# Optimization experiments

Hardware: AMD Instinct MI355X
Metric: run time of the kernel (lower is better)

The kernel has to match this reference:

```python
import jax, jax.numpy as jnp
import numpy as np

T = 8192          # nb_territories
H = 4096          # hidden_size
N_ACT = 65536     # number of possible (orig, dest) action pairs
NEG = -1000.0     # fill value for masked-out actions (matches torch code)


def setup_inputs() -> dict:
    key = jax.random.key(0)
    ks = jax.random.split(key, 8)
    inv_sqrt = lambda n: 1.0 / np.sqrt(n)
    return {
        "possible_actions": jax.random.randint(ks[0], (N_ACT, 2), 0, T, dtype=jnp.int64)
            if jax.config.jax_enable_x64 else jax.random.randint(ks[0], (N_ACT, 2), 0, T, dtype=jnp.int32),
        "player_presence_map": jax.random.normal(ks[1], (T,), dtype=jnp.float32),
        "W_in": jax.random.normal(ks[2], (H, T), dtype=jnp.float32) * inv_sqrt(T),
        "b_in": jax.random.normal(ks[3], (H,), dtype=jnp.float32) * inv_sqrt(T),
        "W_orig": jax.random.normal(ks[4], (T, H), dtype=jnp.float32) * inv_sqrt(H),
        "b_orig": jax.random.normal(ks[5], (T,), dtype=jnp.float32) * inv_sqrt(H),
        "W_dest": jax.random.normal(ks[6], (T, H), dtype=jnp.float32) * inv_sqrt(H),
        "b_dest": jax.random.normal(ks[7], (T,), dtype=jnp.float32) * inv_sqrt(H),
    }


def reference(possible_actions, player_presence_map, W_in, b_in, W_orig, b_orig, W_dest, b_dest):
    # tiny MLP: x = tanh(Linear(presence)); torig/tdest heads
    x = jnp.tanh(W_in @ player_presence_map + b_in)          # [H]
    torig = jnp.tanh(W_orig @ x + b_orig)                    # [T]
    tdest = jnp.tanh(W_dest @ x + b_dest)                    # [T]
    emb = jnp.outer(torig, tdest)                            # [T, T]
    # vectorized scatter replaces the python loop over possible_actions
    mask = jnp.zeros((T, T), dtype=emb.dtype)
    mask = mask.at[possible_actions[:, 0], possible_actions[:, 1]].set(1.0)
    emb = jnp.where(mask == 1.0, emb, jnp.asarray(NEG, emb.dtype))
    logits = emb.reshape(1, T * T)                           # [1, T*T]
    return jax.nn.softmax(logits, axis=1)
```

## Files before the change

kernel.cpp:

```cpp
#include <hip/hip_runtime.h>

constexpr int TT   = 8192;
constexpr int HH   = 4096;
constexpr int NACT = 65536;

__global__ __launch_bounds__(256) void k_gemv_in(
    const float* __restrict__ W, const float* __restrict__ p,
    const float* __restrict__ b, float* __restrict__ x)
{
    const int row = blockIdx.x;
    const int t   = threadIdx.x;
    const float4* __restrict__ Wr = reinterpret_cast<const float4*>(W + (size_t)row * TT);
    const float4* __restrict__ pv = reinterpret_cast<const float4*>(p);
    float acc = 0.f;
#pragma unroll
    for (int i = 0; i < TT / 4 / 256; ++i) {
        float4 w = Wr[i * 256 + t];
        float4 q = pv[i * 256 + t];
        acc += w.x * q.x + w.y * q.y + w.z * q.z + w.w * q.w;
    }
#pragma unroll
    for (int off = 32; off; off >>= 1) acc += __shfl_down(acc, off, 64);
    __shared__ float s[4];
    if ((t & 63) == 0) s[t >> 6] = acc;
    __syncthreads();
    if (t == 0) x[row] = tanhf(s[0] + s[1] + s[2] + s[3] + b[row]);
}

__global__ __launch_bounds__(256) void k_gemv_heads(
    const float* __restrict__ Wo, const float* __restrict__ bo,
    const float* __restrict__ Wd, const float* __restrict__ bd,
    const float* __restrict__ x, float* __restrict__ th)
{
    const int bid = blockIdx.x;
    const int t   = threadIdx.x;
    const float* W; const float* b; int r;
    if (bid < TT) { W = Wo; b = bo; r = bid; }
    else          { W = Wd; b = bd; r = bid - TT; }
    const float4* __restrict__ Wr = reinterpret_cast<const float4*>(W + (size_t)r * HH);
    const float4* __restrict__ xv = reinterpret_cast<const float4*>(x);
    float acc = 0.f;
#pragma unroll
    for (int i = 0; i < HH / 4 / 256; ++i) {
        float4 w = Wr[i * 256 + t];
        float4 q = xv[i * 256 + t];
        acc += w.x * q.x + w.y * q.y + w.z * q.z + w.w * q.w;
    }
#pragma unroll
    for (int off = 32; off; off >>= 1) acc += __shfl_down(acc, off, 64);
    __shared__ float s[4];
    if ((t & 63) == 0) s[t >> 6] = acc;
    __syncthreads();
    if (t == 0) th[bid] = tanhf(s[0] + s[1] + s[2] + s[3] + b[r]);
}

__global__ __launch_bounds__(256) void k_scatter(
    const int* __restrict__ pa, const float* __restrict__ th,
    float* __restrict__ out, float* __restrict__ partial)
{
    const int i = blockIdx.x * 256 + threadIdx.x;
    const int o = pa[2 * i];
    const int d = pa[2 * i + 1];
    const float v = th[o] * th[TT + d];
    const float u = expf(v - 1.0f);
    float old = atomicExch(out + ((size_t)o * TT + d), u);
    float c = (old == 0.0f) ? u : 0.0f;
#pragma unroll
    for (int off = 32; off; off >>= 1) c += __shfl_down(c, off, 64);
    __shared__ float s[4];
    if ((threadIdx.x & 63) == 0) s[threadIdx.x >> 6] = c;
    __syncthreads();
    if (threadIdx.x == 0) partial[blockIdx.x] = s[0] + s[1] + s[2] + s[3];
}

__global__ __launch_bounds__(256) void k_finalize(
    const int* __restrict__ pa, const float* __restrict__ th,
    const float* __restrict__ partial, float* __restrict__ out)
{
    float ps = partial[threadIdx.x];
#pragma unroll
    for (int off = 32; off; off >>= 1) ps += __shfl_down(ps, off, 64);
    __shared__ float s[4];
    __shared__ float invZ;
    if ((threadIdx.x & 63) == 0) s[threadIdx.x >> 6] = ps;
    __syncthreads();
    if (threadIdx.x == 0) invZ = 1.0f / (s[0] + s[1] + s[2] + s[3]);
    __syncthreads();
    const int i = blockIdx.x * 256 + threadIdx.x;
    const int o = pa[2 * i];
    const int d = pa[2 * i + 1];
    const float v = th[o] * th[TT + d];
    out[(size_t)o * TT + d] = expf(v - 1.0f) * invZ;
}

extern "C" void kernel_launch(void* const* d_in, const int* in_sizes, int n_in,
                              void* d_out, int out_size, void* d_ws, size_t ws_size,
                              hipStream_t stream)
{
    const int*   pa  = (const int*)  d_in[0];
    const float* p   = (const float*)d_in[1];
    const float* Win = (const float*)d_in[2];
    const float* bin = (const float*)d_in[3];
    const float* Wo  = (const float*)d_in[4];
    const float* bo  = (const float*)d_in[5];
    const float* Wd  = (const float*)d_in[6];
    const float* bd  = (const float*)d_in[7];
    float* out = (float*)d_out;

    float* x       = (float*)d_ws;
    float* th      = x + HH;
    float* partial = th + 2 * TT;

    hipMemsetAsync(out, 0, (size_t)out_size * sizeof(float), stream);

    k_gemv_in   <<<HH,        256, 0, stream>>>(Win, p, bin, x);
    k_gemv_heads<<<2 * TT,    256, 0, stream>>>(Wo, bo, Wd, bd, x, th);
    k_scatter   <<<NACT / 256, 256, 0, stream>>>(pa, th, out, partial);
    k_finalize  <<<NACT / 256, 256, 0, stream>>>(pa, th, partial, out);
}
```

Baseline: 144.7 us.

## Fuse all stages into one cooperative persistent kernel with grid syncs

Replaces the memset and four kernel launches with a single cooperative kernel that runs each stage in grid-stride loops separated by grid.sync. The output zeroing is folded into the first GEMV phase with nontemporal vector stores, so it can overlap with the W_in reads. This removes launch gaps and the separate memset. The cost is grid-wide barriers, fewer blocks (at most 1024) doing the GEMVs, and host-side occupancy queries on every call. It falls back to the old path if the cooperative launch fails.

```diff
diff --git a/kernel.cpp b/kernel.cpp
--- a/kernel.cpp
+++ b/kernel.cpp
@@ -1,8 +1,116 @@
 #include <hip/hip_runtime.h>
+#include <hip/hip_cooperative_groups.h>
+
+namespace cg = cooperative_groups;
 
 constexpr int TT   = 8192;
 constexpr int HH   = 4096;
 constexpr int NACT = 65536;
+constexpr int NTH  = 256;
+constexpr int NBMAX = 1024;
+
+typedef float f32x4 __attribute__((ext_vector_type(4)));
+
+__device__ __forceinline__ float block_reduce(float v, float* s, int t)
+{
+#pragma unroll
+    for (int off = 32; off; off >>= 1) v += __shfl_down(v, off, 64);
+    if ((t & 63) == 0) s[t >> 6] = v;
+    __syncthreads();
+    float r = s[0] + s[1] + s[2] + s[3];
+    __syncthreads();
+    return r;
+}
+
+__global__ __launch_bounds__(256, 4) void k_fused(
+    const int*   __restrict__ pa,
+    const float* __restrict__ p,
+    const float* __restrict__ Win, const float* __restrict__ bin,
+    const float* __restrict__ Wo,  const float* __restrict__ bo,
+    const float* __restrict__ Wd,  const float* __restrict__ bd,
+    float* __restrict__ out,
+    float* __restrict__ x, float* __restrict__ th, float* __restrict__ partial)
+{
+    cg::grid_group grid = cg::this_grid();
+    const int nb = gridDim.x;
+    const int b  = blockIdx.x;
+    const int t  = threadIdx.x;
+    __shared__ float s[4];
+
+    {
+        const float4* __restrict__ pv = reinterpret_cast<const float4*>(p);
+        for (int row = b; row < HH; row += nb) {
+            const float4* __restrict__ Wr =
+                reinterpret_cast<const float4*>(Win + (size_t)row * TT);
+            float acc = 0.f;
+#pragma unroll
+            for (int i = 0; i < TT / 4 / NTH; ++i) {
+                float4 w = Wr[i * NTH + t];
+                float4 q = pv[i * NTH + t];
+                acc += w.x * q.x + w.y * q.y + w.z * q.z + w.w * q.w;
+            }
+            float sum = block_reduce(acc, s, t);
+            if (t == 0) x[row] = tanhf(sum + bin[row]);
+        }
+        f32x4* __restrict__ o4 = reinterpret_cast<f32x4*>(out);
+        const f32x4 z = {0.f, 0.f, 0.f, 0.f};
+        const int n4 = TT * (TT / 4);
+        const int gstride = nb * NTH;
+        for (int i = b * NTH + t; i < n4; i += gstride)
+            __builtin_nontemporal_store(z, &o4[i]);
+    }
+    grid.sync();
+
+    {
+        const float4* __restrict__ xv = reinterpret_cast<const float4*>(x);
+        for (int r = b; r < 2 * TT; r += nb) {
+            const float* W; const float* bb; int rr;
+            if (r < TT) { W = Wo; bb = bo; rr = r; }
+            else        { W = Wd; bb = bd; rr = r - TT; }
+            const float4* __restrict__ Wr =
+                reinterpret_cast<const float4*>(W + (size_t)rr * HH);
+            float acc = 0.f;
+#pragma unroll
+            for (int i = 0; i < HH / 4 / NTH; ++i) {
+                float4 w = Wr[i * NTH + t];
+                float4 q = xv[i * NTH + t];
+                acc += w.x * q.x + w.y * q.y + w.z * q.z + w.w * q.w;
+            }
+            float sum = block_reduce(acc, s, t);
+            if (t == 0) th[r] = tanhf(sum + bb[rr]);
+        }
+    }
+    grid.sync();
+
+    {
+        float c = 0.f;
+        const int gstride = nb * NTH;
+        for (int i = b * NTH + t; i < NACT; i += gstride) {
+            const int o = pa[2 * i];
+            const int d = pa[2 * i + 1];
+            const float v = th[o] * th[TT + d];
+            const float u = expf(v - 1.0f);
+            float old = atomicExch(out + ((size_t)o * TT + d), u);
+            if (old == 0.0f) c += u;
+        }
+        float bc = block_reduce(c, s, t);
+        if (t == 0) partial[b] = bc;
+    }
+    grid.sync();
+
+    {
+        float ps = 0.f;
+        for (int i = t; i < nb; i += NTH) ps += partial[i];
+        const float invZ = 1.0f / block_reduce(ps, s, t);
+        const int gstride = nb * NTH;
+        for (int i = b * NTH + t; i < NACT; i += gstride) {
+            const int o = pa[2 * i];
+            const int d = pa[2 * i + 1];
+            const float v = th[o] * th[TT + d];
+            out[(size_t)o * TT + d] = expf(v - 1.0f) * invZ;
+        }
+    }
+}
 
 __global__ __launch_bounds__(256) void k_gemv_in(
     const float* __restrict__ W, const float* __restrict__ p,
@@ -19,12 +127,9 @@
         float4 q = pv[i * 256 + t];
         acc += w.x * q.x + w.y * q.y + w.z * q.z + w.w * q.w;
     }
-#pragma unroll
-    for (int off = 32; off; off >>= 1) acc += __shfl_down(acc, off, 64);
-    __shared__ float s[4];
-    if ((t & 63) == 0) s[t >> 6] = acc;
-    __syncthreads();
-    if (t == 0) x[row] = tanhf(s[0] + s[1] + s[2] + s[3] + b[row]);
+    __shared__ float s[4];
+    float sum = block_reduce(acc, s, t);
+    if (t == 0) x[row] = tanhf(sum + b[row]);
 }
 
 __global__ __launch_bounds__(256) void k_gemv_heads(
@@ -46,12 +151,9 @@
         float4 q = xv[i * 256 + t];
         acc += w.x * q.x + w.y * q.y + w.z * q.z + w.w * q.w;
     }
-#pragma unroll
-    for (int off = 32; off; off >>= 1) acc += __shfl_down(acc, off, 64);
-    __shared__ float s[4];
-    if ((t & 63) == 0) s[t >> 6] = acc;
-    __syncthreads();
-    if (t == 0) th[bid] = tanhf(s[0] + s[1] + s[2] + s[3] + b[r]);
+    __shared__ float s[4];
+    float sum = block_reduce(acc, s, t);
+    if (t == 0) th[bid] = tanhf(sum + b[r]);
 }
 
 __global__ __launch_bounds__(256) void k_scatter(
@@ -65,27 +167,17 @@
     const float u = expf(v - 1.0f);
     float old = atomicExch(out + ((size_t)o * TT + d), u);
     float c = (old == 0.0f) ? u : 0.0f;
-#pragma unroll
-    for (int off = 32; off; off >>= 1) c += __shfl_down(c, off, 64);
-    __shared__ float s[4];
-    if ((threadIdx.x & 63) == 0) s[threadIdx.x >> 6] = c;
-    __syncthreads();
-    if (threadIdx.x == 0) partial[blockIdx.x] = s[0] + s[1] + s[2] + s[3];
+    __shared__ float s[4];
+    float bc = block_reduce(c, s, threadIdx.x);
+    if (threadIdx.x == 0) partial[blockIdx.x] = bc;
 }
 
 __global__ __launch_bounds__(256) void k_finalize(
     const int* __restrict__ pa, const float* __restrict__ th,
     const float* __restrict__ partial, float* __restrict__ out)
 {
-    float ps = partial[threadIdx.x];
-#pragma unroll
-    for (int off = 32; off; off >>= 1) ps += __shfl_down(ps, off, 64);
-    __shared__ float s[4];
-    __shared__ float invZ;
-    if ((threadIdx.x & 63) == 0) s[threadIdx.x >> 6] = ps;
-    __syncthreads();
-    if (threadIdx.x == 0) invZ = 1.0f / (s[0] + s[1] + s[2] + s[3]);
-    __syncthreads();
+    __shared__ float s[4];
+    const float invZ = 1.0f / block_reduce(partial[threadIdx.x], s, threadIdx.x);
     const int i = blockIdx.x * 256 + threadIdx.x;
     const int o = pa[2 * i];
     const int d = pa[2 * i + 1];
@@ -111,10 +203,31 @@
     float* th      = x + HH;
     float* partial = th + 2 * TT;
 
-    hipMemsetAsync(out, 0, (size_t)out_size * sizeof(float), stream);
-
-    k_gemv_in   <<<HH,        256, 0, stream>>>(Win, p, bin, x);
-    k_gemv_heads<<<2 * TT,    256, 0, stream>>>(Wo, bo, Wd, bd, x, th);
-    k_scatter   <<<NACT / 256, 256, 0, stream>>>(pa, th, out, partial);
-    k_finalize  <<<NACT / 256, 256, 0, stream>>>(pa, th, partial, out);
-}
+    int dev = 0;
+    (void)hipGetDevice(&dev);
+    int nCU = 0;
+    (void)hipDeviceGetAttribute(&nCU, hipDeviceAttributeMultiprocessorCount, dev);
+    int maxB = 0;
+    (void)hipOccupancyMaxActiveBlocksPerMultiprocessor(&maxB, k_fused, NTH, 0);
+
+    long cap = (long)maxB * (long)nCU;
+    int nb = (cap < NBMAX) ? (int)cap : NBMAX;
+
+    bool coop_ok = false;
+    if (nb >= 64) {
+        void* args[] = { (void*)&pa, (void*)&p, (void*)&Win, (void*)&bin,
+                         (void*)&Wo, (void*)&bo, (void*)&Wd, (void*)&bd,
+                         (void*)&out, (void*)&x, (void*)&th, (void*)&partial };
+        hipError_t le = hipLaunchCooperativeKernel(
+            reinterpret_cast<void*>(k_fused), dim3(nb), dim3(NTH), args, 0, stream);
+        coop_ok = (le == hipSuccess);
+    }
+
+    if (!coop_ok) {
+        hipMemsetAsync(out, 0, (size_t)out_size * sizeof(float), stream);
+        k_gemv_in   <<<HH,         NTH, 0, stream>>>(Win, p, bin, x);
+        k_gemv_heads<<<2 * TT,     NTH, 0, stream>>>(Wo, bo, Wd, bd, x, th);
+        k_scatter   <<<NACT / NTH, NTH, 0, stream>>>(pa, th, out, partial);
+        k_finalize  <<<NACT / NTH, NTH, 0, stream>>>(pa, th, partial, out);
+    }
+}
```

After: 525.8 us. 263% more time.
